# Kernel tuning notes

Measured on AMD Instinct MI355X. Metric: run time of the kernel, lower is better.

Reference implementation:

```python
import jax, jax.numpy as jnp
import numpy as np

B, C, CE, H, W = 4, 128, 64, 64, 64
V = H * W
# parent(i) < i//2 guarantees depth <= ceil(log2(V)) = 12; 14 is a safe static bound
MAX_LEVELS = 14


def _gather_v(x, idx):
    # x: [B, C, V], idx: [B, V] -> gather along vertex dim (broadcast over C)
    return jnp.take_along_axis(x, idx[:, None, :], axis=2)


def _tree_filter(feature_in, embed_in, sorted_index, sorted_parent, node_level):
    Bv, Cv, Hv, Wv = feature_in.shape
    Vv = Hv * Wv
    f = feature_in.reshape(Bv, Cv, Vv)
    e = embed_in.reshape(Bv, embed_in.shape[1], Vv)
    # build_edge_weight: gather to BFS order, gather parent, squared-L2 distance, exp(-d)
    f_s = _gather_v(f, sorted_index)          # [B,C,V] features in topological order
    e_s = _gather_v(e, sorted_index)
    e_p = _gather_v(e_s, sorted_parent)
    d2 = jnp.sum((e_s - e_p) ** 2, axis=1)    # [B,V]
    w = jnp.exp(-d2)                          # edge weight node->parent (root: exp(0)=1, unused)
    wB = w[:, None, :]
    # ---- up sweep (leaves -> root), level-parallel over BFS levels ----
    # A_i = f_i + sum_{c in child(i)} w_c * A_c ; Z_i = 1 + sum w_c * Z_c (self_weight = 1)
    aggr_up = f_s
    nrm_up = jnp.ones((Bv, Vv), feature_in.dtype)
    for d in range(MAX_LEVELS - 1, 0, -1):
        mw = jnp.where(node_level == d, w, jnp.zeros((), feature_in.dtype))
        aggr_up = jax.vmap(lambda a, p, m: a.at[:, p].add(m))(
            aggr_up, sorted_parent, mw[:, None, :] * aggr_up)
        nrm_up = jax.vmap(lambda a, p, m: a.at[p].add(m))(
            nrm_up, sorted_parent, mw * nrm_up)
    # ---- down sweep (root -> leaves) ----
    # Ahat_i = A_i + w_i * (Ahat_parent - w_i * A_i); root keeps A_root
    aggr = aggr_up
    nrm = nrm_up
    for d in range(1, MAX_LEVELS):
        sel = node_level == d
        pa = _gather_v(aggr, sorted_parent)
        aggr = jnp.where(sel[:, None, :], aggr_up + wB * (pa - wB * aggr_up), aggr)
        pn = jnp.take_along_axis(nrm, sorted_parent, axis=1)
        nrm = jnp.where(sel, nrm_up + w * (pn - w * nrm_up), nrm)
    out_s = aggr / nrm[:, None, :]
    # scatter back from BFS order to original vertex order
    out = jax.vmap(lambda o, i: jnp.zeros_like(o).at[:, i].set(o))(out_s, sorted_index)
    return out.reshape(Bv, Cv, Hv, Wv)


def setup_inputs() -> dict:
    key = jax.random.key(0)
    k1, k2 = jax.random.split(key)
    feature_in = jax.random.normal(k1, (B, C, H, W), dtype=jnp.float32)
    embed_in = 0.1 * jax.random.normal(k2, (B, CE, H, W), dtype=jnp.float32)
    rng = np.random.default_rng(0)
    sorted_index = np.stack([rng.permutation(V) for _ in range(B)]).astype(np.int32)
    sorted_parent = np.zeros((B, V), dtype=np.int32)
    node_level = np.zeros((B, V), dtype=np.int32)
    for b in range(B):
        for i in range(1, V):
            p = int(rng.integers(0, max(1, i // 2)))  # parent earlier in order, depth <= log2(V)
            sorted_parent[b, i] = p
            node_level[b, i] = node_level[b, p] + 1
    return {
        "feature_in": feature_in,
        "embed_in": embed_in,
        "sorted_index": jnp.asarray(sorted_index),
        "sorted_parent": jnp.asarray(sorted_parent),
        "node_level": jnp.asarray(node_level),
    }


def reference(feature_in, embed_in, sorted_index, sorted_parent, node_level):
    return _tree_filter(feature_in, embed_in, sorted_index, sorted_parent, node_level)
```

## Files before the change

kernel.cpp:

```cpp
#include <hip/hip_runtime.h>

#define BB 4
#define CC 128
#define CE 64
#define VV 4096
#define NLEV 14


__device__ __forceinline__ void lds_fadd(float* p, float v) {
    unsafeAtomicAdd(p, v);
}

__global__ __launch_bounds__(256) void prep_kernel(
    const float* __restrict__ embed,
    const int* __restrict__ sorted_index,
    const int* __restrict__ sorted_parent,
    const int* __restrict__ node_level,
    int* __restrict__ gi,
    int* __restrict__ gp,
    int* __restrict__ pw,
    int* __restrict__ offs,
    float* __restrict__ et,
    int do_transpose)
{
    int tid = threadIdx.x;
    if (blockIdx.x < BB) {
        int b = blockIdx.x;
        __shared__ int pos_s[VV];
        __shared__ int si_s[VV];
        __shared__ int hist[NLEV + 1];
        __shared__ int cursor[NLEV];
        const int* lev = node_level    + b * VV;
        const int* si  = sorted_index  + b * VV;
        const int* par = sorted_parent + b * VV;

        if (tid < NLEV + 1) hist[tid] = 0;
        __syncthreads();
        for (int i = tid; i < VV; i += 256) {
            si_s[i] = si[i];
            int d = lev[i]; d = d < NLEV - 1 ? d : NLEV - 1;
            atomicAdd(&hist[d], 1);
        }
        __syncthreads();
        if (tid == 0) {
            int acc = 0;
            for (int d = 0; d < NLEV; ++d) { int h = hist[d]; hist[d] = acc; cursor[d] = acc; acc += h; }
            hist[NLEV] = acc;
        }
        __syncthreads();
        if (tid <= NLEV) offs[b * 16 + tid] = hist[tid];
        for (int i = tid; i < VV; i += 256) {
            int d = lev[i]; d = d < NLEV - 1 ? d : NLEV - 1;
            int k = atomicAdd(&cursor[d], 1);
            pos_s[i] = k;
            gi[b * VV + k] = si_s[i];
        }
        __syncthreads();
        for (int i = tid; i < VV; i += 256) {
            int p = par[i];
            int k = pos_s[i];
            pw[b * 2 * VV + 2 * k] = pos_s[p];
            gp[b * VV + k] = si_s[p];
        }
    } else if (do_transpose) {
        int t  = blockIdx.x - BB;
        int b  = t >> 6;
        int v0 = (t & 63) << 6;
        __shared__ float tile[64][65];
        int vloc = tid & 63;
        int ce0  = (tid >> 6) * 16;
        const float* eb = embed + (size_t)b * CE * VV;
        #pragma unroll
        for (int r = 0; r < 16; ++r)
            tile[ce0 + r][vloc] = eb[(size_t)(ce0 + r) * VV + v0 + vloc];
        __syncthreads();
        #pragma unroll
        for (int r = 0; r < 4; ++r) {
            int v  = (tid >> 4) + r * 16;
            int c4 = (tid & 15) * 4;
            float4 val = make_float4(tile[c4][v], tile[c4+1][v], tile[c4+2][v], tile[c4+3][v]);
            *(float4*)(et + ((size_t)(b * VV) + v0 + v) * CE + c4) = val;
        }
    }
}

__global__ __launch_bounds__(256) void weight_t_kernel(
    const float* __restrict__ et,
    const int* __restrict__ gi,
    const int* __restrict__ gp,
    int* __restrict__ pw)
{
    int lane = threadIdx.x & 63;
    int g = blockIdx.x * 4 + (threadIdx.x >> 6);
    int b = g >> 12, k = g & (VV - 1);
    int vi = gi[b * VV + k];
    int vp = gp[b * VV + k];
    float a = et[((size_t)(b * VV) + vi) * CE + lane];
    float q = et[((size_t)(b * VV) + vp) * CE + lane];
    float d = a - q, d2 = d * d;
    #pragma unroll
    for (int o = 32; o > 0; o >>= 1) d2 += __shfl_xor(d2, o, 64);
    if (lane == 0) ((float*)pw)[b * 2 * VV + 2 * k + 1] = __expf(-d2);
}

__global__ __launch_bounds__(256) void weight_s_kernel(
    const float* __restrict__ embed,
    const int* __restrict__ gi,
    const int* __restrict__ gp,
    int* __restrict__ pw)
{
    int lane = threadIdx.x & 63;
    int g = blockIdx.x * 4 + (threadIdx.x >> 6);
    int b = g >> 12, k = g & (VV - 1);
    int vi = gi[b * VV + k];
    int vp = gp[b * VV + k];
    const float* eb = embed + (size_t)b * CE * VV;
    float a = eb[(size_t)lane * VV + vi];
    float q = eb[(size_t)lane * VV + vp];
    float d = a - q, d2 = d * d;
    #pragma unroll
    for (int o = 32; o > 0; o >>= 1) d2 += __shfl_xor(d2, o, 64);
    if (lane == 0) ((float*)pw)[b * 2 * VV + 2 * k + 1] = __expf(-d2);
}

__global__ __launch_bounds__(64) void tree_kernel(
    const float* __restrict__ feat,
    const int* __restrict__ gi,
    const int* __restrict__ pw,
    const int* __restrict__ offs,
    float* __restrict__ out)
{
    __shared__ float vv[2 * VV];
    __shared__ int  pwS[2 * VV];
    int blk  = blockIdx.x;
    int b    = blk >> 7;
    int c    = blk & (CC - 1);
    int lane = threadIdx.x;

    const int*   gB  = gi + b * VV;
    const int*   pwB = pw + b * 2 * VV;
    const int*   off = offs + b * 16;
    const float* f   = feat + ((size_t)(b * CC + c)) * VV;

    #pragma unroll
    for (int t = 0; t < 32; ++t) {
        int4 x = ((const int4*)pwB)[lane + t * 64];
        *(int4*)&pwS[4 * (lane + t * 64)] = x;
    }

    #pragma unroll 8
    for (int k = lane; k < VV; k += 64) {
        int gk = gB[k];
        float2 p; p.x = f[gk]; p.y = 1.0f;
        *(float2*)&vv[2 * k] = p;
    }
    __asm__ volatile("s_waitcnt vmcnt(0) lgkmcnt(0)" ::: "memory");

    for (int d = NLEV - 1; d >= 1; --d) {
        int e = off[d + 1];
        for (int k = off[d] + lane; k < e; k += 64) {
            int2 cw = *(const int2*)&pwS[2 * k];
            int cp = cw.x; float w = __int_as_float(cw.y);
            float2 u = *(const float2*)&vv[2 * k];
            lds_fadd(&vv[2 * cp],     w * u.x);
            lds_fadd(&vv[2 * cp + 1], w * u.y);
        }
        __asm__ volatile("s_waitcnt lgkmcnt(0)" ::: "memory");
    }

    for (int d = 1; d <= NLEV - 1; ++d) {
        int e = off[d + 1];
        for (int k = off[d] + lane; k < e; k += 64) {
            int2 cw = *(const int2*)&pwS[2 * k];
            int cp = cw.x; float w = __int_as_float(cw.y);
            float2 u  = *(const float2*)&vv[2 * k];
            float2 pa = *(const float2*)&vv[2 * cp];
            float2 r;
            r.x = fmaf(w, fmaf(-w, u.x, pa.x), u.x);
            r.y = fmaf(w, fmaf(-w, u.y, pa.y), u.y);
            *(float2*)&vv[2 * k] = r;
        }
        __asm__ volatile("s_waitcnt lgkmcnt(0)" ::: "memory");
    }

    float* ob = out + ((size_t)(b * CC + c)) * VV;
    #pragma unroll 8
    for (int k = lane; k < VV; k += 64) {
        float2 u = *(const float2*)&vv[2 * k];
        ob[gB[k]] = u.x / u.y;
    }
}

extern "C" void kernel_launch(void* const* d_in, const int* in_sizes, int n_in,
                              void* d_out, int out_size, void* d_ws, size_t ws_size,
                              hipStream_t stream) {
    const float* feat          = (const float*)d_in[0];
    const float* embed         = (const float*)d_in[1];
    const int*   sorted_index  = (const int*)d_in[2];
    const int*   sorted_parent = (const int*)d_in[3];
    const int*   node_level    = (const int*)d_in[4];
    float* out = (float*)d_out;

    char* ws = (char*)d_ws;
    const size_t A = (size_t)BB * VV * 4;
    int*   gi   = (int*)(ws);
    int*   gp   = (int*)(ws + A);
    int*   pw   = (int*)(ws + 2 * A);
    int*   offs = (int*)(ws + 4 * A);
    float* et   = (float*)(ws + 4 * A + 4096);
    const size_t need_et = 4 * A + 4096 + (size_t)BB * VV * CE * 4;
    int use_et = (ws_size >= need_et) ? 1 : 0;

    int prep_blocks = use_et ? (BB + BB * 64) : BB;
    prep_kernel<<<prep_blocks, 256, 0, stream>>>(
        embed, sorted_index, sorted_parent, node_level, gi, gp, pw, offs, et, use_et);

    if (use_et)
        weight_t_kernel<<<(BB * VV) / 4, 256, 0, stream>>>(et, gi, gp, pw);
    else
        weight_s_kernel<<<(BB * VV) / 4, 256, 0, stream>>>(embed, gi, gp, pw);

    tree_kernel<<<BB * CC, 64, 0, stream>>>(feat, gi, pw, offs, out);
}
```

Baseline: 127.3 us.

## Use inverse permutation for coalesced I/O and widen tree kernel to 256 threads

Builds an inverse permutation (vertex to sorted position) in the prep kernel so the tree kernel can read features and write outputs with coalesced float4 global accesses, doing the scatter/gather in LDS instead of global memory. The tree kernel grows from one wavefront to 256 threads per block, using __syncthreads between levels instead of a single-wave waitcnt. It also caches level offsets in shared memory and uses fast division. The cost is block-level barriers on every level and lower occupancy per CU from the larger blocks.

```diff
diff --git a/kernel.cpp b/kernel.cpp
--- a/kernel.cpp
+++ b/kernel.cpp
@@ -18,6 +18,7 @@
     const int* __restrict__ node_level,
     int* __restrict__ gi,
     int* __restrict__ gp,
+    int* __restrict__ giInv,
     int* __restrict__ pw,
     int* __restrict__ offs,
     float* __restrict__ et,
@@ -53,7 +54,9 @@
             int d = lev[i]; d = d < NLEV - 1 ? d : NLEV - 1;
             int k = atomicAdd(&cursor[d], 1);
             pos_s[i] = k;
-            gi[b * VV + k] = si_s[i];
+            int v = si_s[i];
+            gi[b * VV + k] = v;
+            giInv[b * VV + v] = k;
         }
         __syncthreads();
         for (int i = tid; i < VV; i += 256) {
@@ -123,71 +126,88 @@
     if (lane == 0) ((float*)pw)[b * 2 * VV + 2 * k + 1] = __expf(-d2);
 }
 
-__global__ __launch_bounds__(64) void tree_kernel(
+__global__ __launch_bounds__(256) void tree_kernel(
     const float* __restrict__ feat,
-    const int* __restrict__ gi,
+    const int* __restrict__ giInv,
     const int* __restrict__ pw,
     const int* __restrict__ offs,
     float* __restrict__ out)
 {
     __shared__ float vv[2 * VV];
     __shared__ int  pwS[2 * VV];
-    int blk  = blockIdx.x;
-    int b    = blk >> 7;
-    int c    = blk & (CC - 1);
-    int lane = threadIdx.x;
-
-    const int*   gB  = gi + b * VV;
-    const int*   pwB = pw + b * 2 * VV;
-    const int*   off = offs + b * 16;
+    __shared__ int  offS[16];
+    int b   = blockIdx.x >> 7;
+    int c   = blockIdx.x & (CC - 1);
+    int tid = threadIdx.x;
+
+    const int*   pwB = pw    + b * 2 * VV;
+    const int*   ivB = giInv + b * VV;
     const float* f   = feat + ((size_t)(b * CC + c)) * VV;
 
-    #pragma unroll
-    for (int t = 0; t < 32; ++t) {
-        int4 x = ((const int4*)pwB)[lane + t * 64];
-        *(int4*)&pwS[4 * (lane + t * 64)] = x;
-    }
-
-    #pragma unroll 8
-    for (int k = lane; k < VV; k += 64) {
-        int gk = gB[k];
-        float2 p; p.x = f[gk]; p.y = 1.0f;
-        *(float2*)&vv[2 * k] = p;
-    }
-    __asm__ volatile("s_waitcnt vmcnt(0) lgkmcnt(0)" ::: "memory");
+    if (tid < 16) offS[tid] = offs[b * 16 + tid];
+
+    #pragma unroll
+    for (int t = 0; t < 8; ++t) {
+        int idx = tid + t * 256;
+        int4 x = ((const int4*)pwB)[idx];
+        *(int4*)&pwS[4 * idx] = x;
+    }
+
+    #pragma unroll
+    for (int t = 0; t < 4; ++t) {
+        int idx = tid + t * 256;
+        float4 fv = ((const float4*)f)[idx];
+        int4   kk = ((const int4*)ivB)[idx];
+        float2 a; a.y = 1.0f;
+        a.x = fv.x; *(float2*)&vv[2 * kk.x] = a;
+        a.x = fv.y; *(float2*)&vv[2 * kk.y] = a;
+        a.x = fv.z; *(float2*)&vv[2 * kk.z] = a;
+        a.x = fv.w; *(float2*)&vv[2 * kk.w] = a;
+    }
+    __syncthreads();
 
     for (int d = NLEV - 1; d >= 1; --d) {
-        int e = off[d + 1];
-        for (int k = off[d] + lane; k < e; k += 64) {
+        int e = offS[d + 1];
+        for (int k = offS[d] + tid; k < e; k += 256) {
             int2 cw = *(const int2*)&pwS[2 * k];
-            int cp = cw.x; float w = __int_as_float(cw.y);
+            float w = __int_as_float(cw.y);
             float2 u = *(const float2*)&vv[2 * k];
-            lds_fadd(&vv[2 * cp],     w * u.x);
-            lds_fadd(&vv[2 * cp + 1], w * u.y);
-        }
-        __asm__ volatile("s_waitcnt lgkmcnt(0)" ::: "memory");
+            lds_fadd(&vv[2 * cw.x],     w * u.x);
+            lds_fadd(&vv[2 * cw.x + 1], w * u.y);
+        }
+        __syncthreads();
     }
 
     for (int d = 1; d <= NLEV - 1; ++d) {
-        int e = off[d + 1];
-        for (int k = off[d] + lane; k < e; k += 64) {
+        int e = offS[d + 1];
+        for (int k = offS[d] + tid; k < e; k += 256) {
             int2 cw = *(const int2*)&pwS[2 * k];
-            int cp = cw.x; float w = __int_as_float(cw.y);
+            float w = __int_as_float(cw.y);
             float2 u  = *(const float2*)&vv[2 * k];
-            float2 pa = *(const float2*)&vv[2 * cp];
+            float2 pa = *(const float2*)&vv[2 * cw.x];
             float2 r;
             r.x = fmaf(w, fmaf(-w, u.x, pa.x), u.x);
             r.y = fmaf(w, fmaf(-w, u.y, pa.y), u.y);
             *(float2*)&vv[2 * k] = r;
         }
-        __asm__ volatile("s_waitcnt lgkmcnt(0)" ::: "memory");
+        __syncthreads();
     }
 
     float* ob = out + ((size_t)(b * CC + c)) * VV;
-    #pragma unroll 8
-    for (int k = lane; k < VV; k += 64) {
-        float2 u = *(const float2*)&vv[2 * k];
-        ob[gB[k]] = u.x / u.y;
+    #pragma unroll
+    for (int t = 0; t < 4; ++t) {
+        int idx = tid + t * 256;
+        int4 kk = ((const int4*)ivB)[idx];
+        float2 u0 = *(const float2*)&vv[2 * kk.x];
+        float2 u1 = *(const float2*)&vv[2 * kk.y];
+        float2 u2 = *(const float2*)&vv[2 * kk.z];
+        float2 u3 = *(const float2*)&vv[2 * kk.w];
+        float4 r;
+        r.x = __fdividef(u0.x, u0.y);
+        r.y = __fdividef(u1.x, u1.y);
+        r.z = __fdividef(u2.x, u2.y);
+        r.w = __fdividef(u3.x, u3.y);
+        ((float4*)ob)[idx] = r;
     }
 }
 
@@ -203,22 +223,24 @@
 
     char* ws = (char*)d_ws;
     const size_t A = (size_t)BB * VV * 4;
-    int*   gi   = (int*)(ws);
-    int*   gp   = (int*)(ws + A);
-    int*   pw   = (int*)(ws + 2 * A);
-    int*   offs = (int*)(ws + 4 * A);
-    float* et   = (float*)(ws + 4 * A + 4096);
-    const size_t need_et = 4 * A + 4096 + (size_t)BB * VV * CE * 4;
+    int*   gi    = (int*)(ws);
+    int*   gp    = (int*)(ws + A);
+    int*   giInv = (int*)(ws + 2 * A);
+    int*   pw    = (int*)(ws + 3 * A);
+    int*   offs  = (int*)(ws + 5 * A);
+    float* et    = (float*)(ws + 5 * A + 4096);
+    const size_t need_et = 5 * A + 4096 + (size_t)BB * VV * CE * 4;
     int use_et = (ws_size >= need_et) ? 1 : 0;
 
     int prep_blocks = use_et ? (BB + BB * 64) : BB;
     prep_kernel<<<prep_blocks, 256, 0, stream>>>(
-        embed, sorted_index, sorted_parent, node_level, gi, gp, pw, offs, et, use_et);
+        embed, sorted_index, sorted_parent, node_level,
+        gi, gp, giInv, pw, offs, et, use_et);
 
     if (use_et)
         weight_t_kernel<<<(BB * VV) / 4, 256, 0, stream>>>(et, gi, gp, pw);
     else
         weight_s_kernel<<<(BB * VV) / 4, 256, 0, stream>>>(embed, gi, gp, pw);
 
-    tree_kernel<<<BB * CC, 64, 0, stream>>>(feat, gi, pw, offs, out);
-}
+    tree_kernel<<<BB * CC, 256, 0, stream>>>(feat, giInv, pw, offs, out);
+}
```

New measurement: 112.2 us. -11.8%, faster.
